# Kernel optimization log

Measured on AMD Instinct MI355X. Metric: run time of the kernel, lower is better.

Reference implementation:

```python
import jax, jax.numpy as jnp
import numpy as np
import math

D_MODEL = 1024
NUM_HEADS = 16
D_K = D_MODEL // NUM_HEADS
B, T = 2, 2048


def setup_inputs() -> dict:
    key = jax.random.key(0)
    ks = jax.random.split(key, 9)
    s = 1.0 / math.sqrt(D_MODEL)
    inp = {
        'x': jax.random.normal(ks[0], (B, T, D_MODEL), dtype=jnp.float32),
        'mask': jnp.tril(jnp.ones((1, 1, T, T), dtype=jnp.int32)),
        'Wq': jax.random.uniform(ks[1], (D_MODEL, D_MODEL), jnp.float32, -s, s),
        'bq': jax.random.uniform(ks[2], (D_MODEL,), jnp.float32, -s, s),
        'Wk': jax.random.uniform(ks[3], (D_MODEL, D_MODEL), jnp.float32, -s, s),
        'bk': jax.random.uniform(ks[4], (D_MODEL,), jnp.float32, -s, s),
        'Wv': jax.random.uniform(ks[5], (D_MODEL, D_MODEL), jnp.float32, -s, s),
        'bv': jax.random.uniform(ks[6], (D_MODEL,), jnp.float32, -s, s),
        'Wo': jax.random.uniform(ks[7], (D_MODEL, D_MODEL), jnp.float32, -s, s),
        'bo': jax.random.uniform(ks[8], (D_MODEL,), jnp.float32, -s, s),
    }
    return inp


def reference(x, mask, Wq, bq, Wk, bk, Wv, bv, Wo, bo):
    Bsz, Tlen, C = x.shape
    # projections; torch Linear computes x @ W.T + b, here W stored as (in,out)-like square so use x @ W + b with W meaning W.T
    q = (x @ Wq + bq).reshape(Bsz, Tlen, NUM_HEADS, D_K).transpose(0, 2, 1, 3)
    k = (x @ Wk + bk).reshape(Bsz, Tlen, NUM_HEADS, D_K).transpose(0, 2, 1, 3)
    v = (x @ Wv + bv).reshape(Bsz, Tlen, NUM_HEADS, D_K).transpose(0, 2, 1, 3)
    scores = jnp.einsum('bhqd,bhkd->bhqk', q, k) / math.sqrt(D_K)  # (B,H,T,T)
    scores = jnp.where(mask == 0, -jnp.inf, scores)
    attn = jax.nn.softmax(scores, axis=-1)
    out = jnp.einsum('bhqk,bhkd->bhqd', attn, v)
    out = out.transpose(0, 2, 1, 3).reshape(Bsz, Tlen, C)
    return out @ Wo + bo
```

## Files before the change

kernel.cpp:

```cpp
#include <hip/hip_runtime.h>
#include <math.h>

typedef unsigned short ushort_t;
typedef short short8 __attribute__((ext_vector_type(8)));
typedef float f32x4 __attribute__((ext_vector_type(4)));

#define DMODEL 1024
#define NHEADS 16
#define DKH    64
#define BATCH  2
#define SEQ    2048
#define BT     (BATCH * SEQ)

__device__ __forceinline__ ushort_t f2bf(float f) {
    union { float f; unsigned u; } a; a.f = f;
    return (ushort_t)((a.u + 0x7FFFu + ((a.u >> 16) & 1u)) >> 16);
}

__device__ __forceinline__ void async_copy16(const ushort_t* g, ushort_t* l) {
    __builtin_amdgcn_global_load_lds(
        (__attribute__((address_space(1))) void*)g,
        (__attribute__((address_space(3))) void*)l, 16, 0, 0);
}

__global__ __launch_bounds__(256) void prep_kernel(
    const float* __restrict__ x, ushort_t* __restrict__ xb,
    const float* __restrict__ Wq, const float* __restrict__ Wk,
    const float* __restrict__ Wv, const float* __restrict__ Wo,
    ushort_t* __restrict__ WqT, ushort_t* __restrict__ WkT,
    ushort_t* __restrict__ WvT, ushort_t* __restrict__ WoT)
{
    __shared__ ushort_t tile[64][72];
    const int bx = blockIdx.x;
    const int tid = threadIdx.x;

    if (bx < 2048) {
        size_t i = ((size_t)bx * 256 + tid) * 8;
        float4 a = *(const float4*)(x + i);
        float4 b = *(const float4*)(x + i + 4);
        union { ushort_t u[8]; short8 v; } r;
        r.u[0] = f2bf(a.x); r.u[1] = f2bf(a.y); r.u[2] = f2bf(a.z); r.u[3] = f2bf(a.w);
        r.u[4] = f2bf(b.x); r.u[5] = f2bf(b.y); r.u[6] = f2bf(b.z); r.u[7] = f2bf(b.w);
        *(short8*)(xb + i) = r.v;
        return;
    }

    const int idx = bx - 2048;
    const int z  = idx >> 8;
    const int n0 = ((idx >> 4) & 15) * 64;
    const int k0 = (idx & 15) * 64;
    const float* W = (z == 0) ? Wq : (z == 1) ? Wk : (z == 2) ? Wv : Wo;
    ushort_t*   WT = (z == 0) ? WqT : (z == 1) ? WkT : (z == 2) ? WvT : WoT;

    const int r  = tid >> 2;
    const int cb = (tid & 3) * 16;
#pragma unroll
    for (int u = 0; u < 4; ++u) {
        float4 v = *(const float4*)(W + (size_t)(k0 + r) * DMODEL + n0 + cb + u * 4);
        union { ushort_t u4[4]; unsigned long long ll; } p;
        p.u4[0] = f2bf(v.x); p.u4[1] = f2bf(v.y); p.u4[2] = f2bf(v.z); p.u4[3] = f2bf(v.w);
        *(unsigned long long*)&tile[r][cb + u * 4] = p.ll;
    }
    __syncthreads();
    const int n  = tid >> 2;
    const int kb = (tid & 3) * 16;
#pragma unroll
    for (int half = 0; half < 2; ++half) {
        union { ushort_t u8[8]; short8 v; } p;
#pragma unroll
        for (int j = 0; j < 8; ++j) p.u8[j] = tile[kb + half * 8 + j][n];
        *(short8*)(WT + (size_t)(n0 + n) * DMODEL + k0 + kb + half * 8) = p.v;
    }
}

__global__ __launch_bounds__(512, 2) void qkv_gemm(
    const ushort_t* __restrict__ xb,
    const ushort_t* __restrict__ WqT, const ushort_t* __restrict__ WkT,
    const ushort_t* __restrict__ WvT,
    const float* __restrict__ bq, const float* __restrict__ bk,
    const float* __restrict__ bv,
    ushort_t* __restrict__ Qb, ushort_t* __restrict__ Kb, ushort_t* __restrict__ VTo)
{
    __shared__ ushort_t As[2 * 16384];
    __shared__ ushort_t Bs[2 * 16384];

    const int tid  = threadIdx.x;
    const int wid  = tid >> 6, lane = tid & 63;
    const int l15  = lane & 15, quad = lane >> 4;
    const int wm   = wid >> 2, wn = wid & 3;
    const int m0   = blockIdx.x * 256;
    const int n0g  = blockIdx.y * 256;
    const int z    = n0g >> 10;
    const ushort_t* WT = (z == 0) ? WqT : (z == 1) ? WkT : WvT;
    const float* bias  = (z == 0) ? bq : (z == 1) ? bk : bv;

    const ushort_t* Abase = xb + (size_t)m0 * DMODEL;
    const ushort_t* Bbase = WT + (size_t)(n0g & 1023) * DMODEL;

    const int srow = lane >> 3;
    const int scol = ((lane & 7) ^ srow) << 3;
    const int swz  = l15 & 7;

    auto STAGE = [&](int t, int e) {
        const int buf = t & 1;
        const int h   = e & 1;
        const int k0  = t * 64;
        ushort_t* dst = ((e < 2) ? As : Bs) + buf * 16384;
        const ushort_t* src = (e < 2) ? Abase : Bbase;
#pragma unroll
        for (int c = 0; c < 2; ++c) {
            int ch = h * 16 + wid * 2 + c;
            async_copy16(src + (size_t)(ch * 8 + srow) * DMODEL + k0 + scol,
                         dst + ch * 512);
        }
    };

    f32x4 acc[8][4];
    const f32x4 zero = {0.f, 0.f, 0.f, 0.f};
#pragma unroll
    for (int i = 0; i < 8; ++i)
#pragma unroll
        for (int j = 0; j < 4; ++j) acc[i][j] = zero;

#pragma unroll
    for (int e = 0; e < 4; ++e) STAGE(0, e);
    asm volatile("s_waitcnt vmcnt(0)" ::: "memory");
    __builtin_amdgcn_s_barrier();
    __builtin_amdgcn_sched_barrier(0);

    for (int j = 0; j < 8; ++j) {
#pragma unroll
        for (int half = 0; half < 2; ++half) {
            const int t   = 2 * j + half;
            const int buf = half;
            const ushort_t* Ab = As + buf * 16384;
            const ushort_t* Bb = Bs + buf * 16384;
            const int ts  = t + 1;
            const bool dostage = (ts < 16);

            short8 bfr[4];
#pragma unroll
            for (int ph = 0; ph < 4; ++ph) {
                const int kk = ph >> 1, mh = ph & 1;

                if (ph == 0) {
                    if (dostage) {
                        STAGE(ts, 0);
                        asm volatile("s_waitcnt vmcnt(2)" ::: "memory");
                    } else {
                        asm volatile("s_waitcnt vmcnt(0)" ::: "memory");
                    }
                    __builtin_amdgcn_s_barrier();
                    __builtin_amdgcn_sched_barrier(0);
                }

                if (mh == 0) {
#pragma unroll
                    for (int n = 0; n < 4; ++n) {
                        int rb = wn * 64 + n * 16 + l15;
                        bfr[n] = *(const short8*)(Bb + rb * 64 +
                                                  (((kk * 4 + quad) ^ swz) << 3));
                    }
                }
                short8 af[4];
#pragma unroll
                for (int i = 0; i < 4; ++i) {
                    int m = mh * 4 + i;
                    int ra = wm * 128 + m * 16 + l15;
                    af[i] = *(const short8*)(Ab + ra * 64 +
                                             (((kk * 4 + quad) ^ swz) << 3));
                }

                if (ph != 0) {
                    if (dostage) STAGE(ts, ph);
                    __builtin_amdgcn_s_barrier();
                }

                asm volatile("s_waitcnt lgkmcnt(0)" ::: "memory");
                __builtin_amdgcn_sched_barrier(0);
                __builtin_amdgcn_s_setprio(1);
#pragma unroll
                for (int i = 0; i < 4; ++i) {
                    int m = mh * 4 + i;
#pragma unroll
                    for (int n = 0; n < 4; ++n)
                        acc[m][n] = __builtin_amdgcn_mfma_f32_16x16x32_bf16(
                            af[i], bfr[n], acc[m][n], 0, 0, 0);
                }
                __builtin_amdgcn_s_setprio(0);
                __builtin_amdgcn_s_barrier();
            }
        }
    }

    float bcol[4];
#pragma unroll
    for (int n = 0; n < 4; ++n)
        bcol[n] = bias[(n0g & 1023) + wn * 64 + n * 16 + l15];

    if (z == 2) {
#pragma unroll
        for (int m = 0; m < 8; ++m) {
            int row0 = m0 + wm * 128 + m * 16 + quad * 4;
            int b = row0 >> 11, trow = row0 & (SEQ - 1);
            int tb = trow & ~63;
            int idxp = ((m & 1) << 2) | (quad << 3) | (((m >> 1) & 1) << 5);
#pragma unroll
            for (int n = 0; n < 4; ++n) {
                int colz = (n0g & 1023) + wn * 64 + n * 16 + l15;
                int h = colz >> 6, d = colz & 63;
                union { ushort_t u4[4]; unsigned long long ll; } pk;
#pragma unroll
                for (int reg = 0; reg < 4; ++reg)
                    pk.u4[reg] = f2bf(acc[m][n][reg] + bcol[n]);
                *(unsigned long long*)(VTo +
                    ((size_t)(b * NHEADS + h) * DKH + d) * SEQ + tb + idxp) = pk.ll;
            }
        }
    } else {
        ushort_t* out = (z == 0) ? Qb : Kb;
#pragma unroll
        for (int m = 0; m < 8; ++m)
#pragma unroll
            for (int reg = 0; reg < 4; ++reg) {
                int row = m0 + wm * 128 + m * 16 + quad * 4 + reg;
                int b = row >> 11, trow = row & (SEQ - 1);
#pragma unroll
                for (int n = 0; n < 4; ++n) {
                    int colz = (n0g & 1023) + wn * 64 + n * 16 + l15;
                    int h = colz >> 6, d = colz & 63;
                    out[((((size_t)b * NHEADS + h) * SEQ + trow) << 6) + d] =
                        f2bf(acc[m][n][reg] + bcol[n]);
                }
            }
    }
}

__device__ __forceinline__ void gemm_dbuf_m64(
    const ushort_t* __restrict__ A, const ushort_t* __restrict__ B,
    int m0, int n0, ushort_t* At, ushort_t* Bt, f32x4 (&acc)[2][4])
{
    const int tid  = threadIdx.x;
    const int w    = tid >> 6, lane = tid & 63;
    const int l15  = lane & 15, quad = lane >> 4;
    const int wm   = w & 1, wn = w >> 1;
    const int srow = lane >> 3;
    const int scol = ((lane & 7) ^ srow) << 3;
    const int swz  = l15 & 7;

#pragma unroll
    for (int c = 0; c < 2; ++c) {
        int ch = w * 2 + c;
        async_copy16(A + (size_t)(m0 + ch * 8 + srow) * DMODEL + scol, At + ch * 512);
    }
#pragma unroll
    for (int c = 0; c < 4; ++c) {
        int ch = w * 4 + c;
        async_copy16(B + (size_t)(n0 + ch * 8 + srow) * DMODEL + scol, Bt + ch * 512);
    }
    __syncthreads();

    for (int kt = 0; kt < DMODEL / 64; ++kt) {
        const int curA = (kt & 1) << 12;
        const int curB = (kt & 1) << 13;
        if (kt + 1 < DMODEL / 64) {
            const int k0 = (kt + 1) * 64;
#pragma unroll
            for (int c = 0; c < 2; ++c) {
                int ch = w * 2 + c;
                async_copy16(A + (size_t)(m0 + ch * 8 + srow) * DMODEL + k0 + scol,
                             At + (curA ^ 4096) + ch * 512);
            }
#pragma unroll
            for (int c = 0; c < 4; ++c) {
                int ch = w * 4 + c;
                async_copy16(B + (size_t)(n0 + ch * 8 + srow) * DMODEL + k0 + scol,
                             Bt + (curB ^ 8192) + ch * 512);
            }
        }
#pragma unroll
        for (int kk = 0; kk < 2; ++kk) {
            short8 af[2], bf[4];
#pragma unroll
            for (int t = 0; t < 2; ++t) {
                int ra = wm * 32 + t * 16 + l15;
                af[t] = *(const short8*)(At + curA + ra * 64 +
                                         (((kk * 4 + quad) ^ swz) << 3));
            }
#pragma unroll
            for (int t = 0; t < 4; ++t) {
                int rb = wn * 64 + t * 16 + l15;
                bf[t] = *(const short8*)(Bt + curB + rb * 64 +
                                         (((kk * 4 + quad) ^ swz) << 3));
            }
#pragma unroll
            for (int mt = 0; mt < 2; ++mt)
#pragma unroll
                for (int nt = 0; nt < 4; ++nt)
                    acc[mt][nt] = __builtin_amdgcn_mfma_f32_16x16x32_bf16(
                        af[mt], bf[nt], acc[mt][nt], 0, 0, 0);
        }
        __syncthreads();
    }
}

__global__ __launch_bounds__(256) void attn_kernel(
    const ushort_t* __restrict__ Qb, const ushort_t* __restrict__ Kb,
    const ushort_t* __restrict__ VT, ushort_t* __restrict__ AO)
{
    const int bi = blockIdx.x;
    const int bh = bi & 31;
    const int b  = bh >> 4, h = bh & 15;
    const int qq = bi >> 5;
    const int tid = threadIdx.x, w = tid >> 6, lane = tid & 63;
    const int l15 = lane & 15, quad = lane >> 4;

    __shared__ ushort_t Kt[2][64 * 64];
    __shared__ ushort_t Vt[2][64 * 64];

    const ushort_t* Kbase = Kb + (((size_t)bh * SEQ) << 6);
    const ushort_t* Vbase = VT + (size_t)bh * DKH * SEQ;

    const int srow = lane >> 3;
    const int schx = (lane & 7) ^ srow;
    const int swz  = l15 & 7;
    const f32x4 zero = {0.f, 0.f, 0.f, 0.f};
    const float cexp = 0.18033688011112042f;

    union { ushort_t u8[8]; short8 v; } ones;
#pragma unroll
    for (int j = 0; j < 8; ++j) ones.u8[j] = 0x3F80;

    for (int job = 0; job < 2; ++job) {
        const int qt = job ? (31 - qq) : qq;
        const int q0 = qt * 64;
        const int nk = qt + 1;

        short8 qa[2];
#pragma unroll
        for (int ks = 0; ks < 2; ++ks)
            qa[ks] = *(const short8*)(
                Qb + (((size_t)bh * SEQ + q0 + w * 16 + l15) << 6) + ks * 32 + quad * 8);

        f32x4 lacc = zero;
        f32x4 o[4];
#pragma unroll
        for (int dt = 0; dt < 4; ++dt) o[dt] = zero;

#pragma unroll
        for (int c = 0; c < 2; ++c) {
            int chunk = w * 2 + c;
            async_copy16(Kbase + (((size_t)(chunk * 8 + srow)) << 6) + schx * 8,
                         &Kt[0][chunk * 512]);
            async_copy16(Vbase + (size_t)(chunk * 8 + srow) * SEQ + schx * 8,
                         &Vt[0][chunk * 512]);
        }
        __syncthreads();

        for (int kt = 0; kt < nk; ++kt) {
            const int buf = kt & 1;
            if (kt + 1 < nk) {
                const int kt0n = (kt + 1) * 64;
#pragma unroll
                for (int c = 0; c < 2; ++c) {
                    int chunk = w * 2 + c;
                    async_copy16(Kbase + (((size_t)(kt0n + chunk * 8 + srow)) << 6) + schx * 8,
                                 &Kt[buf ^ 1][chunk * 512]);
                    async_copy16(Vbase + (size_t)(chunk * 8 + srow) * SEQ + kt0n + schx * 8,
                                 &Vt[buf ^ 1][chunk * 512]);
                }
            }

            short8 kf[4][2], vf[2][4];
#pragma unroll
            for (int kt_i = 0; kt_i < 4; ++kt_i)
#pragma unroll
                for (int ks = 0; ks < 2; ++ks)
                    kf[kt_i][ks] = *(const short8*)&Kt[buf][(kt_i * 16 + l15) * 64 +
                                                            (((ks * 4 + quad) ^ swz) << 3)];
#pragma unroll
            for (int g = 0; g < 2; ++g)
#pragma unroll
                for (int dt = 0; dt < 4; ++dt)
                    vf[g][dt] = *(const short8*)&Vt[buf][(dt * 16 + l15) * 64 +
                                                         ((((g << 2) | quad) ^ swz) << 3)];

            f32x4 sc[4];
#pragma unroll
            for (int kt_i = 0; kt_i < 4; ++kt_i) sc[kt_i] = zero;
#pragma unroll
            for (int ks = 0; ks < 2; ++ks)
#pragma unroll
                for (int kt_i = 0; kt_i < 4; ++kt_i)
                    sc[kt_i] = __builtin_amdgcn_mfma_f32_16x16x32_bf16(
                        kf[kt_i][ks], qa[ks], sc[kt_i], 0, 0, 0);

            const bool domask = (kt == qt);
            const int qabs = q0 + w * 16 + l15;
            unsigned pka[4], pkb[4];
#pragma unroll
            for (int kt_i = 0; kt_i < 4; ++kt_i) {
                float p[4];
#pragma unroll
                for (int r = 0; r < 4; ++r) {
                    float pv = exp2f(cexp * sc[kt_i][r]);
                    if (domask && (kt * 64 + kt_i * 16 + quad * 4 + r) > qabs) pv = 0.f;
                    p[r] = pv;
                }
                pka[kt_i] = __builtin_amdgcn_perm(
                    __float_as_uint(p[1]), __float_as_uint(p[0]), 0x07060302u);
                pkb[kt_i] = __builtin_amdgcn_perm(
                    __float_as_uint(p[3]), __float_as_uint(p[2]), 0x07060302u);
            }

#pragma unroll
            for (int g = 0; g < 2; ++g) {
                union { unsigned u[4]; short8 v; } pf;
                pf.u[0] = pka[2 * g];
                pf.u[1] = pkb[2 * g];
                pf.u[2] = pka[2 * g + 1];
                pf.u[3] = pkb[2 * g + 1];
                lacc = __builtin_amdgcn_mfma_f32_16x16x32_bf16(
                    pf.v, ones.v, lacc, 0, 0, 0);
#pragma unroll
                for (int dt = 0; dt < 4; ++dt)
                    o[dt] = __builtin_amdgcn_mfma_f32_16x16x32_bf16(
                        pf.v, vf[g][dt], o[dt], 0, 0, 0);
            }

            __syncthreads();
        }

#pragma unroll
        for (int r = 0; r < 4; ++r) {
            float inv = 1.0f / lacc[r];
            int t = q0 + w * 16 + quad * 4 + r;
#pragma unroll
            for (int dt = 0; dt < 4; ++dt)
                AO[((size_t)b * SEQ + t) * DMODEL + h * 64 + dt * 16 + l15] =
                    f2bf(o[dt][r] * inv);
        }
    }
}

__global__ __launch_bounds__(256) void out_gemm(
    const ushort_t* __restrict__ AO, const ushort_t* __restrict__ WoT,
    const float* __restrict__ bo, float* __restrict__ out)
{
    __shared__ ushort_t At[2 * 4096];
    __shared__ ushort_t Bt[2 * 8192];
    const int m0 = blockIdx.x * 64, n0 = blockIdx.y * 128;

    f32x4 zero = {0.f, 0.f, 0.f, 0.f};
    f32x4 acc[2][4];
#pragma unroll
    for (int i = 0; i < 2; ++i)
#pragma unroll
        for (int j = 0; j < 4; ++j) acc[i][j] = zero;

    gemm_dbuf_m64(AO, WoT, m0, n0, At, Bt, acc);

    const int tid = threadIdx.x, w = tid >> 6, lane = tid & 63;
    const int l15 = lane & 15, quad = lane >> 4;
    const int wm = w & 1, wn = w >> 1;

    float bcol[4];
#pragma unroll
    for (int nt = 0; nt < 4; ++nt) bcol[nt] = bo[n0 + wn * 64 + nt * 16 + l15];

#pragma unroll
    for (int mt = 0; mt < 2; ++mt)
#pragma unroll
        for (int reg = 0; reg < 4; ++reg) {
            int row = m0 + wm * 32 + mt * 16 + quad * 4 + reg;
#pragma unroll
            for (int nt = 0; nt < 4; ++nt) {
                int col = n0 + wn * 64 + nt * 16 + l15;
                out[(size_t)row * DMODEL + col] = acc[mt][nt][reg] + bcol[nt];
            }
        }
}

extern "C" void kernel_launch(void* const* d_in, const int* in_sizes, int n_in,
                              void* d_out, int out_size, void* d_ws, size_t ws_size,
                              hipStream_t stream)
{
    const float* x  = (const float*)d_in[0];
    const float* Wq = (const float*)d_in[2];
    const float* bq = (const float*)d_in[3];
    const float* Wk = (const float*)d_in[4];
    const float* bk = (const float*)d_in[5];
    const float* Wv = (const float*)d_in[6];
    const float* bv = (const float*)d_in[7];
    const float* Wo = (const float*)d_in[8];
    const float* bo = (const float*)d_in[9];
    float* out = (float*)d_out;

    ushort_t* ws = (ushort_t*)d_ws;
    size_t off = 0;
    ushort_t* xb  = ws + off; off += (size_t)BT * DMODEL;
    ushort_t* WqT = ws + off; off += (size_t)DMODEL * DMODEL;
    ushort_t* WkT = ws + off; off += (size_t)DMODEL * DMODEL;
    ushort_t* WvT = ws + off; off += (size_t)DMODEL * DMODEL;
    ushort_t* WoT = ws + off; off += (size_t)DMODEL * DMODEL;
    ushort_t* Qb  = ws + off; off += (size_t)BT * DMODEL;
    ushort_t* Kb  = ws + off; off += (size_t)BT * DMODEL;
    ushort_t* VTb = ws + off; off += (size_t)BT * DMODEL;
    ushort_t* AOb = ws + off; off += (size_t)BT * DMODEL;

    prep_kernel<<<2048 + 1024, 256, 0, stream>>>(
        x, xb, Wq, Wk, Wv, Wo, WqT, WkT, WvT, WoT);
    qkv_gemm<<<dim3(BT / 256, 3 * DMODEL / 256), 512, 0, stream>>>(
        xb, WqT, WkT, WvT, bq, bk, bv, Qb, Kb, VTb);
    attn_kernel<<<dim3(SEQ / 64 * NHEADS * BATCH / 2), 256, 0, stream>>>(
        Qb, Kb, VTb, AOb);
    out_gemm<<<dim3(BT / 64, DMODEL / 128), 256, 0, stream>>>(
        AOb, WoT, bo, out);
}
```

Measured before the change: 195.4 us.

## Split paired attention jobs into one block per query tile, fold scale into Q

The attention kernel now launches one block per 64-row query tile instead of pairing a short and a long tile per block, ordering blocks longest-first. The softmax scale (log2e/sqrt(dk)) is folded into Q in the QKV GEMM epilogue, so the attention inner loop calls the raw hardware exp2 with no multiply. The causal mask check moves into a separate branch that runs only on the diagonal tile. MFMA sections are wrapped in s_setprio to favour matrix issue. The split doubles the grid, relying on the hardware scheduler for load balance where the pairing previously did it by hand. Rounding Q to bf16 after scaling changes precision slightly.

```diff
diff --git a/kernel.cpp b/kernel.cpp
--- a/kernel.cpp
+++ b/kernel.cpp
@@ -218,6 +218,7 @@
             }
         }
     } else {
+        const float qs = (z == 0) ? 0.18033688011112042f : 1.0f;
         ushort_t* out = (z == 0) ? Qb : Kb;
 #pragma unroll
         for (int m = 0; m < 8; ++m)
@@ -230,7 +231,7 @@
                     int colz = (n0g & 1023) + wn * 64 + n * 16 + l15;
                     int h = colz >> 6, d = colz & 63;
                     out[((((size_t)b * NHEADS + h) * SEQ + trow) << 6) + d] =
-                        f2bf(acc[m][n][reg] + bcol[n]);
+                        f2bf((acc[m][n][reg] + bcol[n]) * qs);
                 }
             }
     }
@@ -311,7 +312,7 @@
     const int bi = blockIdx.x;
     const int bh = bi & 31;
     const int b  = bh >> 4, h = bh & 15;
-    const int qq = bi >> 5;
+    const int qt = 31 - (bi >> 5);
     const int tid = threadIdx.x, w = tid >> 6, lane = tid & 63;
     const int l15 = lane & 15, quad = lane >> 4;
 
@@ -325,86 +326,85 @@
     const int schx = (lane & 7) ^ srow;
     const int swz  = l15 & 7;
     const f32x4 zero = {0.f, 0.f, 0.f, 0.f};
-    const float cexp = 0.18033688011112042f;
 
     union { ushort_t u8[8]; short8 v; } ones;
 #pragma unroll
     for (int j = 0; j < 8; ++j) ones.u8[j] = 0x3F80;
 
-    for (int job = 0; job < 2; ++job) {
-        const int qt = job ? (31 - qq) : qq;
-        const int q0 = qt * 64;
-        const int nk = qt + 1;
-
-        short8 qa[2];
+    const int q0 = qt * 64;
+    const int nk = qt + 1;
+    const int rq = w * 16 + l15;
+
+    short8 qa[2];
+#pragma unroll
+    for (int ks = 0; ks < 2; ++ks)
+        qa[ks] = *(const short8*)(
+            Qb + (((size_t)bh * SEQ + q0 + w * 16 + l15) << 6) + ks * 32 + quad * 8);
+
+    f32x4 lacc = zero;
+    f32x4 o[4];
+#pragma unroll
+    for (int dt = 0; dt < 4; ++dt) o[dt] = zero;
+
+#pragma unroll
+    for (int c = 0; c < 2; ++c) {
+        int chunk = w * 2 + c;
+        async_copy16(Kbase + (((size_t)(chunk * 8 + srow)) << 6) + schx * 8,
+                     &Kt[0][chunk * 512]);
+        async_copy16(Vbase + (size_t)(chunk * 8 + srow) * SEQ + schx * 8,
+                     &Vt[0][chunk * 512]);
+    }
+    __syncthreads();
+
+    for (int kt = 0; kt < nk; ++kt) {
+        const int buf = kt & 1;
+        if (kt + 1 < nk) {
+            const int kt0n = (kt + 1) * 64;
+#pragma unroll
+            for (int c = 0; c < 2; ++c) {
+                int chunk = w * 2 + c;
+                async_copy16(Kbase + (((size_t)(kt0n + chunk * 8 + srow)) << 6) + schx * 8,
+                             &Kt[buf ^ 1][chunk * 512]);
+                async_copy16(Vbase + (size_t)(chunk * 8 + srow) * SEQ + kt0n + schx * 8,
+                             &Vt[buf ^ 1][chunk * 512]);
+            }
+        }
+
+        short8 kf[4][2], vf[2][4];
+#pragma unroll
+        for (int kt_i = 0; kt_i < 4; ++kt_i)
+#pragma unroll
+            for (int ks = 0; ks < 2; ++ks)
+                kf[kt_i][ks] = *(const short8*)&Kt[buf][(kt_i * 16 + l15) * 64 +
+                                                        (((ks * 4 + quad) ^ swz) << 3)];
+#pragma unroll
+        for (int g = 0; g < 2; ++g)
+#pragma unroll
+            for (int dt = 0; dt < 4; ++dt)
+                vf[g][dt] = *(const short8*)&Vt[buf][(dt * 16 + l15) * 64 +
+                                                     ((((g << 2) | quad) ^ swz) << 3)];
+
+        f32x4 sc[4];
+#pragma unroll
+        for (int kt_i = 0; kt_i < 4; ++kt_i) sc[kt_i] = zero;
+        __builtin_amdgcn_s_setprio(1);
 #pragma unroll
         for (int ks = 0; ks < 2; ++ks)
-            qa[ks] = *(const short8*)(
-                Qb + (((size_t)bh * SEQ + q0 + w * 16 + l15) << 6) + ks * 32 + quad * 8);
-
-        f32x4 lacc = zero;
-        f32x4 o[4];
-#pragma unroll
-        for (int dt = 0; dt < 4; ++dt) o[dt] = zero;
-
-#pragma unroll
-        for (int c = 0; c < 2; ++c) {
-            int chunk = w * 2 + c;
-            async_copy16(Kbase + (((size_t)(chunk * 8 + srow)) << 6) + schx * 8,
-                         &Kt[0][chunk * 512]);
-            async_copy16(Vbase + (size_t)(chunk * 8 + srow) * SEQ + schx * 8,
-                         &Vt[0][chunk * 512]);
-        }
-        __syncthreads();
-
-        for (int kt = 0; kt < nk; ++kt) {
-            const int buf = kt & 1;
-            if (kt + 1 < nk) {
-                const int kt0n = (kt + 1) * 64;
-#pragma unroll
-                for (int c = 0; c < 2; ++c) {
-                    int chunk = w * 2 + c;
-                    async_copy16(Kbase + (((size_t)(kt0n + chunk * 8 + srow)) << 6) + schx * 8,
-                                 &Kt[buf ^ 1][chunk * 512]);
-                    async_copy16(Vbase + (size_t)(chunk * 8 + srow) * SEQ + kt0n + schx * 8,
-                                 &Vt[buf ^ 1][chunk * 512]);
-                }
-            }
-
-            short8 kf[4][2], vf[2][4];
 #pragma unroll
             for (int kt_i = 0; kt_i < 4; ++kt_i)
-#pragma unroll
-                for (int ks = 0; ks < 2; ++ks)
-                    kf[kt_i][ks] = *(const short8*)&Kt[buf][(kt_i * 16 + l15) * 64 +
-                                                            (((ks * 4 + quad) ^ swz) << 3)];
-#pragma unroll
-            for (int g = 0; g < 2; ++g)
-#pragma unroll
-                for (int dt = 0; dt < 4; ++dt)
-                    vf[g][dt] = *(const short8*)&Vt[buf][(dt * 16 + l15) * 64 +
-                                                         ((((g << 2) | quad) ^ swz) << 3)];
-
-            f32x4 sc[4];
-#pragma unroll
-            for (int kt_i = 0; kt_i < 4; ++kt_i) sc[kt_i] = zero;
-#pragma unroll
-            for (int ks = 0; ks < 2; ++ks)
-#pragma unroll
-                for (int kt_i = 0; kt_i < 4; ++kt_i)
-                    sc[kt_i] = __builtin_amdgcn_mfma_f32_16x16x32_bf16(
-                        kf[kt_i][ks], qa[ks], sc[kt_i], 0, 0, 0);
-
-            const bool domask = (kt == qt);
-            const int qabs = q0 + w * 16 + l15;
-            unsigned pka[4], pkb[4];
+                sc[kt_i] = __builtin_amdgcn_mfma_f32_16x16x32_bf16(
+                    kf[kt_i][ks], qa[ks], sc[kt_i], 0, 0, 0);
+        __builtin_amdgcn_s_setprio(0);
+
+        unsigned pka[4], pkb[4];
+        if (kt == qt) {
 #pragma unroll
             for (int kt_i = 0; kt_i < 4; ++kt_i) {
                 float p[4];
 #pragma unroll
                 for (int r = 0; r < 4; ++r) {
-                    float pv = exp2f(cexp * sc[kt_i][r]);
-                    if (domask && (kt * 64 + kt_i * 16 + quad * 4 + r) > qabs) pv = 0.f;
+                    float pv = __builtin_amdgcn_exp2f(sc[kt_i][r]);
+                    if ((kt_i * 16 + quad * 4 + r) > rq) pv = 0.f;
                     p[r] = pv;
                 }
                 pka[kt_i] = __builtin_amdgcn_perm(
@@ -412,34 +412,48 @@
                 pkb[kt_i] = __builtin_amdgcn_perm(
                     __float_as_uint(p[3]), __float_as_uint(p[2]), 0x07060302u);
             }
-
-#pragma unroll
-            for (int g = 0; g < 2; ++g) {
-                union { unsigned u[4]; short8 v; } pf;
-                pf.u[0] = pka[2 * g];
-                pf.u[1] = pkb[2 * g];
-                pf.u[2] = pka[2 * g + 1];
-                pf.u[3] = pkb[2 * g + 1];
-                lacc = __builtin_amdgcn_mfma_f32_16x16x32_bf16(
-                    pf.v, ones.v, lacc, 0, 0, 0);
-#pragma unroll
-                for (int dt = 0; dt < 4; ++dt)
-                    o[dt] = __builtin_amdgcn_mfma_f32_16x16x32_bf16(
-                        pf.v, vf[g][dt], o[dt], 0, 0, 0);
-            }
-
-            __syncthreads();
-        }
-
-#pragma unroll
-        for (int r = 0; r < 4; ++r) {
-            float inv = 1.0f / lacc[r];
-            int t = q0 + w * 16 + quad * 4 + r;
+        } else {
+#pragma unroll
+            for (int kt_i = 0; kt_i < 4; ++kt_i) {
+                float p[4];
+#pragma unroll
+                for (int r = 0; r < 4; ++r)
+                    p[r] = __builtin_amdgcn_exp2f(sc[kt_i][r]);
+                pka[kt_i] = __builtin_amdgcn_perm(
+                    __float_as_uint(p[1]), __float_as_uint(p[0]), 0x07060302u);
+                pkb[kt_i] = __builtin_amdgcn_perm(
+                    __float_as_uint(p[3]), __float_as_uint(p[2]), 0x07060302u);
+            }
+        }
+
+        __builtin_amdgcn_s_setprio(1);
+#pragma unroll
+        for (int g = 0; g < 2; ++g) {
+            union { unsigned u[4]; short8 v; } pf;
+            pf.u[0] = pka[2 * g];
+            pf.u[1] = pkb[2 * g];
+            pf.u[2] = pka[2 * g + 1];
+            pf.u[3] = pkb[2 * g + 1];
+            lacc = __builtin_amdgcn_mfma_f32_16x16x32_bf16(
+                pf.v, ones.v, lacc, 0, 0, 0);
 #pragma unroll
             for (int dt = 0; dt < 4; ++dt)
-                AO[((size_t)b * SEQ + t) * DMODEL + h * 64 + dt * 16 + l15] =
-                    f2bf(o[dt][r] * inv);
-        }
+                o[dt] = __builtin_amdgcn_mfma_f32_16x16x32_bf16(
+                    pf.v, vf[g][dt], o[dt], 0, 0, 0);
+        }
+        __builtin_amdgcn_s_setprio(0);
+
+        __syncthreads();
+    }
+
+#pragma unroll
+    for (int r = 0; r < 4; ++r) {
+        float inv = 1.0f / lacc[r];
+        int t = q0 + w * 16 + quad * 4 + r;
+#pragma unroll
+        for (int dt = 0; dt < 4; ++dt)
+            AO[((size_t)b * SEQ + t) * DMODEL + h * 64 + dt * 16 + l15] =
+                f2bf(o[dt][r] * inv);
     }
 }
 
@@ -512,7 +526,7 @@
         x, xb, Wq, Wk, Wv, Wo, WqT, WkT, WvT, WoT);
     qkv_gemm<<<dim3(BT / 256, 3 * DMODEL / 256), 512, 0, stream>>>(
         xb, WqT, WkT, WvT, bq, bk, bv, Qb, Kb, VTb);
-    attn_kernel<<<dim3(SEQ / 64 * NHEADS * BATCH / 2), 256, 0, stream>>>(
+    attn_kernel<<<dim3(SEQ / 64 * NHEADS * BATCH), 256, 0, stream>>>(
         Qb, Kb, VTb, AOb);
     out_gemm<<<dim3(BT / 64, DMODEL / 128), 256, 0, stream>>>(
         AOb, WoT, bo, out);
```

After: 184.4 us. 1.06x faster.
